# Optimization experiments

Hardware: AMD Instinct MI355X
Metric: run time of the kernel (lower is better)

## Reference

```python
import jax, jax.numpy as jnp
import numpy as np

TOPK = 50

def setup_inputs() -> dict:
    key = jax.random.key(0)
    k1, k2, k3, k4 = jax.random.split(key, 4)
    B, C, H, W = 8, 64, 256, 256
    x = jax.random.normal(k1, (B, C, H, W), dtype=jnp.float32)
    w_qkv = jax.random.normal(k2, (3 * C, C), dtype=jnp.float32) * 0.05
    w_proj = jax.random.normal(k3, (C, C), dtype=jnp.float32) * 0.05
    b_proj = jax.random.normal(k4, (C,), dtype=jnp.float32) * 0.05
    return {"x": x, "w_qkv": w_qkv, "w_proj": w_proj, "b_proj": b_proj}

def reference(x, w_qkv, w_proj, b_proj):
    B, C, H, W = x.shape
    N = H * W
    scale = C ** -0.5  # num_heads = 1, head_dim = C
    # NOTE: torch does x.reshape(B, N, C) on a (B,C,H,W) tensor -> raw
    # row-major reinterpretation; jnp.reshape matches this exactly.
    xf = x.reshape(B, N, C)
    qkv = xf @ w_qkv.T                                # (B, N, 3C)
    qkv = qkv.reshape(B, N, 3, 1, C).transpose(2, 0, 3, 1, 4)
    q, k, v = qkv[0], qkv[1], qkv[2]                  # each (B, 1, N, C)
    # channel attention: v^T @ k -> (B, 1, C, C)
    attn = jnp.einsum('bhnc,bhnd->bhcd', v, k) * scale
    # top-k mask along last dim (scatter of ones at top-k indices)
    _, idx = jax.lax.top_k(attn, TOPK)                # (B, 1, C, TOPK)
    mask = jax.nn.one_hot(idx, C, dtype=jnp.bool_).any(axis=-2)  # (B,1,C,C)
    attn = jnp.where(mask, attn, -jnp.inf)
    attn = jax.nn.softmax(attn, axis=-1)
    # attn @ q^T -> (B, 1, C, N), then raw reshape to (B, N, C) as in torch
    out = jnp.einsum('bhcd,bhnd->bhcn', attn, q).reshape(B, N, C)
    out = out @ w_proj.T + b_proj
    return out.reshape(B, C, H, W) + x
```

## Files before the change

kernel.cpp:

```cpp
#include <hip/hip_runtime.h>
#include <hip/hip_bf16.h>


#define BATCHES 8
#define NROWS 65536
#define CDIM 64
#define BATCH_FLOATS (NROWS * CDIM)

typedef __attribute__((ext_vector_type(8))) short bf16x8;
typedef __attribute__((ext_vector_type(4))) float f32x4;

__device__ __forceinline__ short f2bf(float f) {
    union { __hip_bfloat16 h; short s; } u;
    u.h = __float2bfloat16(f);
    return u.s;
}
__device__ __forceinline__ unsigned int pk2(float a, float b) {
    return (unsigned int)(unsigned short)f2bf(a) |
           ((unsigned int)(unsigned short)f2bf(b) << 16);
}

__device__ __forceinline__ void fma16g(float a, const float* __restrict__ p, float* acc) {
#pragma unroll
    for (int k = 0; k < 16; ++k) acc[k] = fmaf(a, p[k], acc[k]);
}
__device__ __forceinline__ void fma16v(float a, const float4* p, float* acc) {
    float4 b0 = p[0], b1 = p[1], b2 = p[2], b3 = p[3];
    acc[0]  = fmaf(a, b0.x, acc[0]);  acc[1]  = fmaf(a, b0.y, acc[1]);
    acc[2]  = fmaf(a, b0.z, acc[2]);  acc[3]  = fmaf(a, b0.w, acc[3]);
    acc[4]  = fmaf(a, b1.x, acc[4]);  acc[5]  = fmaf(a, b1.y, acc[5]);
    acc[6]  = fmaf(a, b1.z, acc[6]);  acc[7]  = fmaf(a, b1.w, acc[7]);
    acc[8]  = fmaf(a, b2.x, acc[8]);  acc[9]  = fmaf(a, b2.y, acc[9]);
    acc[10] = fmaf(a, b2.z, acc[10]); acc[11] = fmaf(a, b2.w, acc[11]);
    acc[12] = fmaf(a, b3.x, acc[12]); acc[13] = fmaf(a, b3.y, acc[13]);
    acc[14] = fmaf(a, b3.z, acc[14]); acc[15] = fmaf(a, b3.w, acc[15]);
}

__global__ __launch_bounds__(256) void k1_gram(const float* __restrict__ x,
                                               float* __restrict__ Gpart,
                                               int ntiles) {
    __shared__ __align__(16) short xt[2][64 * 72];
    int p = blockIdx.x, b = blockIdx.y;
    int tid = threadIdx.x;
    int l = tid & 63;
    int w = tid >> 6;
    int lm = l & 15, q = l >> 4;
    int n0 = 4 * (tid >> 4);
    int c0 = tid & 15;
    const float* xb = x + (size_t)b * BATCH_FLOATS + (size_t)p * ntiles * 4096;

    f32x4 acc[4];
#pragma unroll
    for (int mi = 0; mi < 4; ++mi) acc[mi] = (f32x4){0.f, 0.f, 0.f, 0.f};

    float pre[4][4];
#pragma unroll
    for (int r = 0; r < 4; ++r)
#pragma unroll
        for (int i = 0; i < 4; ++i)
            pre[r][i] = xb[(size_t)(n0 + r) * 64 + c0 + 16 * i];

    for (int tt = 0; tt < ntiles; ++tt) {
        short* buf = xt[tt & 1];
#pragma unroll
        for (int i = 0; i < 4; ++i) {
            int f = c0 + 16 * i;
            uint2 pk;
            pk.x = pk2(pre[0][i], pre[1][i]);
            pk.y = pk2(pre[2][i], pre[3][i]);
            *(uint2*)&buf[f * 72 + n0] = pk;
        }
        if (tt + 1 < ntiles) {
            const float* nx = xb + (size_t)(tt + 1) * 4096;
#pragma unroll
            for (int r = 0; r < 4; ++r)
#pragma unroll
                for (int i = 0; i < 4; ++i)
                    pre[r][i] = nx[(size_t)(n0 + r) * 64 + c0 + 16 * i];
        }
        __syncthreads();
        bf16x8 bfrag[2];
#pragma unroll
        for (int ks = 0; ks < 2; ++ks)
            bfrag[ks] = *(const bf16x8*)&buf[(16 * w + lm) * 72 + ks * 32 + q * 8];
#pragma unroll
        for (int mi = 0; mi < 4; ++mi) {
#pragma unroll
            for (int ks = 0; ks < 2; ++ks) {
                bf16x8 af = *(const bf16x8*)&buf[(mi * 16 + lm) * 72 + ks * 32 + q * 8];
                acc[mi] = __builtin_amdgcn_mfma_f32_16x16x32_bf16(af, bfrag[ks], acc[mi], 0, 0, 0);
            }
        }
    }
    float* Gp = Gpart + ((size_t)(b * 64 + p) << 12);
#pragma unroll
    for (int mi = 0; mi < 4; ++mi)
#pragma unroll
        for (int r = 0; r < 4; ++r)
            Gp[(mi * 16 + q * 4 + r) * 64 + 16 * w + lm] = acc[mi][r];
}

#define S68 68
__global__ __launch_bounds__(256) void k2_attn(const float* __restrict__ Gpart,
                                               const float* __restrict__ w_qkv,
                                               const float* __restrict__ w_proj,
                                               ushort* __restrict__ m_bf,
                                               ushort* __restrict__ wpb) {
    __shared__ float A[64 * S68];
    __shared__ float Bf[64 * S68];
    __shared__ float Cf[64 * S68];
    int b = blockIdx.x;
    int tid = threadIdx.x;
    int lane = tid & 63;
    int w = __builtin_amdgcn_readfirstlane(tid >> 6);

    if (tid < 128) {
        int idx = b * 128 + tid;
        float4 v = ((const float4*)w_proj)[idx];
        uint2 pp;
        pp.x = pk2(v.x, v.y);
        pp.y = pk2(v.z, v.w);
        *(uint2*)(wpb + 4 * idx) = pp;
    }

    {
        const float* gp = Gpart + ((size_t)b * 64 << 12);
        float4 s[4];
#pragma unroll
        for (int u = 0; u < 4; ++u) s[u] = make_float4(0.f, 0.f, 0.f, 0.f);
#pragma unroll 4
        for (int p = 0; p < 64; ++p) {
            const float4* g4 = (const float4*)(gp + ((size_t)p << 12));
#pragma unroll
            for (int u = 0; u < 4; ++u) {
                float4 v = g4[u * 256 + tid];
                s[u].x += v.x; s[u].y += v.y; s[u].z += v.z; s[u].w += v.w;
            }
        }
#pragma unroll
        for (int u = 0; u < 4; ++u) {
            int idx = u * 256 + tid;
            int c = idx >> 4, f = (idx & 15) * 4;
            A[c * S68 + f + 0] = s[u].x; A[c * S68 + f + 1] = s[u].y;
            A[c * S68 + f + 2] = s[u].z; A[c * S68 + f + 3] = s[u].w;
        }
    }
#pragma unroll
    for (int u = 0; u < 4; ++u) {
        int idx = u * 256 + tid;
        int d = idx >> 4, f = (idx & 15) * 4;
        float4 kv = ((const float4*)(w_qkv + 64 * 64))[idx];
        Bf[(f + 0) * S68 + d] = kv.x; Bf[(f + 1) * S68 + d] = kv.y;
        Bf[(f + 2) * S68 + d] = kv.z; Bf[(f + 3) * S68 + d] = kv.w;
        float4 vv = ((const float4*)(w_qkv + 128 * 64))[idx];
        Cf[(f + 0) * S68 + d] = vv.x; Cf[(f + 1) * S68 + d] = vv.y;
        Cf[(f + 2) * S68 + d] = vv.z; Cf[(f + 3) * S68 + d] = vv.w;
    }
    __syncthreads();

    float acc[16];
#pragma unroll
    for (int k = 0; k < 16; ++k) acc[k] = 0.f;
    for (int f = 0; f < 64; ++f)
        fma16v(A[f * S68 + lane], (const float4*)&Bf[f * S68 + 16 * w], acc);
    __syncthreads();
#pragma unroll
    for (int k = 0; k < 16; ++k) A[lane * S68 + 16 * w + k] = acc[k];
    __syncthreads();

#pragma unroll
    for (int k = 0; k < 16; ++k) acc[k] = 0.f;
    for (int e = 0; e < 64; ++e)
        fma16v(Cf[e * S68 + lane], (const float4*)&A[e * S68 + 16 * w], acc);
#pragma unroll
    for (int k = 0; k < 16; ++k) Bf[lane * S68 + 16 * w + k] = acc[k] * 0.125f;
    __syncthreads();

#pragma unroll 1
    for (int k = 0; k < 16; ++k) {
        int c = 16 * w + k;
        float v = Bf[c * S68 + lane];
        int rank = 0;
#pragma unroll
        for (int d4 = 0; d4 < 16; ++d4) {
            float4 vv = *(const float4*)&Bf[c * S68 + 4 * d4];
            rank += (vv.x > v) || (vv.x == v && (4 * d4 + 0) < lane);
            rank += (vv.y > v) || (vv.y == v && (4 * d4 + 1) < lane);
            rank += (vv.z > v) || (vv.z == v && (4 * d4 + 2) < lane);
            rank += (vv.w > v) || (vv.w == v && (4 * d4 + 3) < lane);
        }
        bool act = rank < 50;
        float mv = act ? v : -INFINITY;
#pragma unroll
        for (int s = 1; s < 64; s <<= 1) mv = fmaxf(mv, __shfl_xor(mv, s, 64));
        float e = act ? expf(v - mv) : 0.f;
        float sum = e;
#pragma unroll
        for (int s = 1; s < 64; s <<= 1) sum += __shfl_xor(sum, s, 64);
        Cf[lane * S68 + c] = e / sum;
    }
    __syncthreads();

#pragma unroll
    for (int k = 0; k < 16; ++k) acc[k] = 0.f;
    for (int d = 0; d < 64; ++d)
        fma16g(Cf[d * S68 + lane], w_qkv + d * 64 + 16 * w, acc);
    unsigned int uu[8];
#pragma unroll
    for (int i = 0; i < 8; ++i)
        uu[i] = pk2(acc[2 * i], acc[2 * i + 1]);
    ushort* dst = m_bf + (size_t)b * 4096 + lane * 64 + 16 * w;
    *(uint4*)dst = make_uint4(uu[0], uu[1], uu[2], uu[3]);
    *(uint4*)(dst + 8) = make_uint4(uu[4], uu[5], uu[6], uu[7]);
}

__global__ __launch_bounds__(256) void k3_main(const float* __restrict__ x,
                                               const ushort* __restrict__ m_bf,
                                               const ushort* __restrict__ wpb,
                                               const float* __restrict__ b_proj,
                                               float* __restrict__ out) {
    __shared__ __align__(16) short xt[64 * 64];
    __shared__ __align__(16) short yyt[64 * 64];
    int t = blockIdx.x, b = blockIdx.y;
    int tid = threadIdx.x;
    int l = tid & 63;
    int w = tid >> 6;
    int lm = l & 15, q = l >> 4;
    const float* xb = x + (size_t)b * BATCH_FLOATS;

    int rowbase = (16 * w + lm) * 1024 + t;
    const float* xr = xb + (size_t)rowbase * 64 + q * 4;
    float4 resid[4];
#pragma unroll
    for (int mi = 0; mi < 4; ++mi) resid[mi] = *(const float4*)(xr + mi * 16);

    const ushort* mb = m_bf + (size_t)b * 4096;
    bf16x8 b1[2];
#pragma unroll
    for (int ks = 0; ks < 2; ++ks)
        b1[ks] = *(const bf16x8*)(mb + (16 * w + lm) * 64 + ks * 32 + q * 8);

    {
        const float4* s = (const float4*)(xb + (size_t)(64 * t) * 64);
#pragma unroll
        for (int u = 0; u < 4; ++u) {
            float4 v = s[u * 256 + tid];
            int row = u * 16 + (tid >> 4);
            int colb = (tid & 15) * 8;
            int off = row * 128 + (colb ^ ((row & 7) << 4));
            uint2 p;
            p.x = pk2(v.x, v.y);
            p.y = pk2(v.z, v.w);
            *(uint2*)((char*)xt + off) = p;
        }
    }
    __syncthreads();

    f32x4 acc1[4];
#pragma unroll
    for (int mi = 0; mi < 4; ++mi) {
        acc1[mi] = (f32x4){0.f, 0.f, 0.f, 0.f};
#pragma unroll
        for (int ks = 0; ks < 2; ++ks) {
            int row = mi * 16 + lm;
            bf16x8 af = *(const bf16x8*)((const char*)xt + row * 128 +
                                         ((ks * 64 + q * 16) ^ ((lm & 7) << 4)));
            acc1[mi] = __builtin_amdgcn_mfma_f32_16x16x32_bf16(af, b1[ks], acc1[mi], 0, 0, 0);
        }
    }
    {
        int r = 16 * w + lm;
#pragma unroll
        for (int mi = 0; mi < 4; ++mi) {
            uint2 p;
            p.x = pk2(acc1[mi][0], acc1[mi][1]);
            p.y = pk2(acc1[mi][2], acc1[mi][3]);
            int off = r * 128 + (((mi * 32) + (q * 8)) ^ ((r & 7) << 4));
            *(uint2*)((char*)yyt + off) = p;
        }
    }

    bf16x8 b2[2];
    {
        int r = 16 * w + lm;
#pragma unroll
        for (int ks = 0; ks < 2; ++ks)
            b2[ks] = *(const bf16x8*)((const char*)yyt + r * 128 +
                                      ((ks * 64 + q * 16) ^ ((r & 7) << 4)));
    }
    f32x4 acc2[4];
#pragma unroll
    for (int mi = 0; mi < 4; ++mi) {
        acc2[mi] = (f32x4){0.f, 0.f, 0.f, 0.f};
#pragma unroll
        for (int ks = 0; ks < 2; ++ks) {
            bf16x8 af = *(const bf16x8*)(wpb + (mi * 16 + lm) * 64 + ks * 32 + q * 8);
            acc2[mi] = __builtin_amdgcn_mfma_f32_16x16x32_bf16(af, b2[ks], acc2[mi], 0, 0, 0);
        }
    }

    float* ob = out + (size_t)b * BATCH_FLOATS + (size_t)rowbase * 64 + q * 4;
#pragma unroll
    for (int mi = 0; mi < 4; ++mi) {
        float4 bias = *(const float4*)(b_proj + mi * 16 + q * 4);
        float4 o;
        o.x = acc2[mi][0] + bias.x + resid[mi].x;
        o.y = acc2[mi][1] + bias.y + resid[mi].y;
        o.z = acc2[mi][2] + bias.z + resid[mi].z;
        o.w = acc2[mi][3] + bias.w + resid[mi].w;
        *(float4*)(ob + mi * 16) = o;
    }
}

extern "C" void kernel_launch(void* const* d_in, const int* in_sizes, int n_in,
                              void* d_out, int out_size, void* d_ws, size_t ws_size,
                              hipStream_t stream) {
    (void)in_sizes; (void)n_in; (void)out_size; (void)ws_size;
    const float* x      = (const float*)d_in[0];
    const float* w_qkv  = (const float*)d_in[1];
    const float* w_proj = (const float*)d_in[2];
    const float* b_proj = (const float*)d_in[3];
    float* out = (float*)d_out;
    float* ws  = (float*)d_ws;

    float*  Gpart = ws;
    ushort* m_bf  = (ushort*)(ws + 8 * 64 * 4096);
    ushort* wpb   = m_bf + 8 * 4096;

    k1_gram<<<dim3(64, BATCHES), 256, 0, stream>>>(x, Gpart, 16);
    k2_attn<<<BATCHES, 256, 0, stream>>>(Gpart, w_qkv, w_proj, m_bf, wpb);
    k3_main<<<dim3(1024, BATCHES), 256, 0, stream>>>(x, m_bf, wpb, b_proj, out);
}
```

Measured before the change: 361.6 us.

## Compute Q projection in gram kernel and split Gpart reduction into separate kernel

Result: slower. 386.3 us (+6.8%).

```diff
diff --git a/kernel.cpp b/kernel.cpp
--- a/kernel.cpp
+++ b/kernel.cpp
@@ -20,10 +20,6 @@
            ((unsigned int)(unsigned short)f2bf(b) << 16);
 }
 
-__device__ __forceinline__ void fma16g(float a, const float* __restrict__ p, float* acc) {
-#pragma unroll
-    for (int k = 0; k < 16; ++k) acc[k] = fmaf(a, p[k], acc[k]);
-}
 __device__ __forceinline__ void fma16v(float a, const float4* p, float* acc) {
     float4 b0 = p[0], b1 = p[1], b2 = p[2], b3 = p[3];
     acc[0]  = fmaf(a, b0.x, acc[0]);  acc[1]  = fmaf(a, b0.y, acc[1]);
@@ -37,9 +33,12 @@
 }
 
 __global__ __launch_bounds__(256) void k1_gram(const float* __restrict__ x,
+                                               const float* __restrict__ w_qkv,
                                                float* __restrict__ Gpart,
+                                               ushort* __restrict__ Qw,
                                                int ntiles) {
     __shared__ __align__(16) short xt[2][64 * 72];
+    __shared__ __align__(16) short xr[2][64 * 72];
     int p = blockIdx.x, b = blockIdx.y;
     int tid = threadIdx.x;
     int l = tid & 63;
@@ -48,6 +47,18 @@
     int n0 = 4 * (tid >> 4);
     int c0 = tid & 15;
     const float* xb = x + (size_t)b * BATCH_FLOATS + (size_t)p * ntiles * 4096;
+    ushort* Qb = Qw + (size_t)b * BATCH_FLOATS + (size_t)p * ntiles * 4096;
+
+    bf16x8 wqf[2];
+#pragma unroll
+    for (int ks = 0; ks < 2; ++ks) {
+        const float* wp = w_qkv + (16 * w + lm) * 64 + ks * 32 + q * 8;
+        float4 a0 = *(const float4*)wp, a1 = *(const float4*)(wp + 4);
+        bf16x8 f;
+        f[0] = f2bf(a0.x); f[1] = f2bf(a0.y); f[2] = f2bf(a0.z); f[3] = f2bf(a0.w);
+        f[4] = f2bf(a1.x); f[5] = f2bf(a1.y); f[6] = f2bf(a1.z); f[7] = f2bf(a1.w);
+        wqf[ks] = f;
+    }
 
     f32x4 acc[4];
 #pragma unroll
@@ -62,6 +73,7 @@
 
     for (int tt = 0; tt < ntiles; ++tt) {
         short* buf = xt[tt & 1];
+        short* bufr = xr[tt & 1];
 #pragma unroll
         for (int i = 0; i < 4; ++i) {
             int f = c0 + 16 * i;
@@ -69,6 +81,9 @@
             pk.x = pk2(pre[0][i], pre[1][i]);
             pk.y = pk2(pre[2][i], pre[3][i]);
             *(uint2*)&buf[f * 72 + n0] = pk;
+#pragma unroll
+            for (int r = 0; r < 4; ++r)
+                bufr[(n0 + r) * 72 + f] = f2bf(pre[r][i]);
         }
         if (tt + 1 < ntiles) {
             const float* nx = xb + (size_t)(tt + 1) * 4096;
@@ -91,6 +106,19 @@
                 acc[mi] = __builtin_amdgcn_mfma_f32_16x16x32_bf16(af, bfrag[ks], acc[mi], 0, 0, 0);
             }
         }
+#pragma unroll
+        for (int mi = 0; mi < 4; ++mi) {
+            f32x4 aq = (f32x4){0.f, 0.f, 0.f, 0.f};
+#pragma unroll
+            for (int ks = 0; ks < 2; ++ks) {
+                bf16x8 af = *(const bf16x8*)&bufr[(mi * 16 + lm) * 72 + ks * 32 + q * 8];
+                aq = __builtin_amdgcn_mfma_f32_16x16x32_bf16(af, wqf[ks], aq, 0, 0, 0);
+            }
+            ushort* qd = Qb + (size_t)(tt * 64 + mi * 16 + q * 4) * 64 + 16 * w + lm;
+#pragma unroll
+            for (int r = 0; r < 4; ++r)
+                qd[r * 64] = (ushort)f2bf(aq[r]);
+        }
     }
     float* Gp = Gpart + ((size_t)(b * 64 + p) << 12);
 #pragma unroll
@@ -100,11 +128,22 @@
             Gp[(mi * 16 + q * 4 + r) * 64 + 16 * w + lm] = acc[mi][r];
 }
 
+__global__ __launch_bounds__(256) void k1b_reduce(const float* __restrict__ Gpart,
+                                                  float* __restrict__ G) {
+    int b = blockIdx.y;
+    int e = blockIdx.x * 256 + threadIdx.x;
+    const float* gp = Gpart + ((size_t)(b * 64) << 12) + e;
+    float s = 0.f;
+#pragma unroll 8
+    for (int pp = 0; pp < 64; ++pp) s += gp[(size_t)pp << 12];
+    G[b * 4096 + e] = s;
+}
+
 #define S68 68
-__global__ __launch_bounds__(256) void k2_attn(const float* __restrict__ Gpart,
+__global__ __launch_bounds__(256) void k2_attn(const float* __restrict__ G,
                                                const float* __restrict__ w_qkv,
                                                const float* __restrict__ w_proj,
-                                               ushort* __restrict__ m_bf,
+                                               ushort* __restrict__ a_bf,
                                                ushort* __restrict__ wpb) {
     __shared__ float A[64 * S68];
     __shared__ float Bf[64 * S68];
@@ -124,25 +163,14 @@
     }
 
     {
-        const float* gp = Gpart + ((size_t)b * 64 << 12);
-        float4 s[4];
-#pragma unroll
-        for (int u = 0; u < 4; ++u) s[u] = make_float4(0.f, 0.f, 0.f, 0.f);
-#pragma unroll 4
-        for (int p = 0; p < 64; ++p) {
-            const float4* g4 = (const float4*)(gp + ((size_t)p << 12));
-#pragma unroll
-            for (int u = 0; u < 4; ++u) {
-                float4 v = g4[u * 256 + tid];
-                s[u].x += v.x; s[u].y += v.y; s[u].z += v.z; s[u].w += v.w;
-            }
-        }
+        const float4* g4 = (const float4*)(G + b * 4096);
 #pragma unroll
         for (int u = 0; u < 4; ++u) {
             int idx = u * 256 + tid;
             int c = idx >> 4, f = (idx & 15) * 4;
-            A[c * S68 + f + 0] = s[u].x; A[c * S68 + f + 1] = s[u].y;
-            A[c * S68 + f + 2] = s[u].z; A[c * S68 + f + 3] = s[u].w;
+            float4 g = g4[idx];
+            A[c * S68 + f + 0] = g.x; A[c * S68 + f + 1] = g.y;
+            A[c * S68 + f + 2] = g.z; A[c * S68 + f + 3] = g.w;
         }
     }
 #pragma unroll
@@ -176,6 +204,7 @@
     for (int k = 0; k < 16; ++k) Bf[lane * S68 + 16 * w + k] = acc[k] * 0.125f;
     __syncthreads();
 
+    ushort* ab = a_bf + (size_t)b * 4096;
 #pragma unroll 1
     for (int k = 0; k < 16; ++k) {
         int c = 16 * w + k;
@@ -197,29 +226,16 @@
         float sum = e;
 #pragma unroll
         for (int s = 1; s < 64; s <<= 1) sum += __shfl_xor(sum, s, 64);
-        Cf[lane * S68 + c] = e / sum;
-    }
-    __syncthreads();
-
-#pragma unroll
-    for (int k = 0; k < 16; ++k) acc[k] = 0.f;
-    for (int d = 0; d < 64; ++d)
-        fma16g(Cf[d * S68 + lane], w_qkv + d * 64 + 16 * w, acc);
-    unsigned int uu[8];
-#pragma unroll
-    for (int i = 0; i < 8; ++i)
-        uu[i] = pk2(acc[2 * i], acc[2 * i + 1]);
-    ushort* dst = m_bf + (size_t)b * 4096 + lane * 64 + 16 * w;
-    *(uint4*)dst = make_uint4(uu[0], uu[1], uu[2], uu[3]);
-    *(uint4*)(dst + 8) = make_uint4(uu[4], uu[5], uu[6], uu[7]);
+        ab[c * 64 + lane] = (ushort)f2bf(e / sum);
+    }
 }
 
 __global__ __launch_bounds__(256) void k3_main(const float* __restrict__ x,
-                                               const ushort* __restrict__ m_bf,
+                                               const ushort* __restrict__ Qw,
+                                               const ushort* __restrict__ a_bf,
                                                const ushort* __restrict__ wpb,
                                                const float* __restrict__ b_proj,
                                                float* __restrict__ out) {
-    __shared__ __align__(16) short xt[64 * 64];
     __shared__ __align__(16) short yyt[64 * 64];
     int t = blockIdx.x, b = blockIdx.y;
     int tid = threadIdx.x;
@@ -234,37 +250,20 @@
 #pragma unroll
     for (int mi = 0; mi < 4; ++mi) resid[mi] = *(const float4*)(xr + mi * 16);
 
-    const ushort* mb = m_bf + (size_t)b * 4096;
+    const ushort* ab = a_bf + (size_t)b * 4096;
     bf16x8 b1[2];
 #pragma unroll
     for (int ks = 0; ks < 2; ++ks)
-        b1[ks] = *(const bf16x8*)(mb + (16 * w + lm) * 64 + ks * 32 + q * 8);
-
-    {
-        const float4* s = (const float4*)(xb + (size_t)(64 * t) * 64);
-#pragma unroll
-        for (int u = 0; u < 4; ++u) {
-            float4 v = s[u * 256 + tid];
-            int row = u * 16 + (tid >> 4);
-            int colb = (tid & 15) * 8;
-            int off = row * 128 + (colb ^ ((row & 7) << 4));
-            uint2 p;
-            p.x = pk2(v.x, v.y);
-            p.y = pk2(v.z, v.w);
-            *(uint2*)((char*)xt + off) = p;
-        }
-    }
-    __syncthreads();
-
+        b1[ks] = *(const bf16x8*)(ab + (16 * w + lm) * 64 + ks * 32 + q * 8);
+
+    const ushort* Qt = Qw + (size_t)b * BATCH_FLOATS + (size_t)(64 * t) * 64;
     f32x4 acc1[4];
 #pragma unroll
     for (int mi = 0; mi < 4; ++mi) {
         acc1[mi] = (f32x4){0.f, 0.f, 0.f, 0.f};
 #pragma unroll
         for (int ks = 0; ks < 2; ++ks) {
-            int row = mi * 16 + lm;
-            bf16x8 af = *(const bf16x8*)((const char*)xt + row * 128 +
-                                         ((ks * 64 + q * 16) ^ ((lm & 7) << 4)));
+            bf16x8 af = *(const bf16x8*)(Qt + (size_t)(mi * 16 + lm) * 64 + ks * 32 + q * 8);
             acc1[mi] = __builtin_amdgcn_mfma_f32_16x16x32_bf16(af, b1[ks], acc1[mi], 0, 0, 0);
         }
     }
@@ -321,13 +320,16 @@
     const float* w_proj = (const float*)d_in[2];
     const float* b_proj = (const float*)d_in[3];
     float* out = (float*)d_out;
-    float* ws  = (float*)d_ws;
-
-    float*  Gpart = ws;
-    ushort* m_bf  = (ushort*)(ws + 8 * 64 * 4096);
-    ushort* wpb   = m_bf + 8 * 4096;
-
-    k1_gram<<<dim3(64, BATCHES), 256, 0, stream>>>(x, Gpart, 16);
-    k2_attn<<<BATCHES, 256, 0, stream>>>(Gpart, w_qkv, w_proj, m_bf, wpb);
-    k3_main<<<dim3(1024, BATCHES), 256, 0, stream>>>(x, m_bf, wpb, b_proj, out);
-}
+    char*  ws  = (char*)d_ws;
+
+    float*  Gpart = (float*)(ws);
+    ushort* Qw    = (ushort*)(ws + (8u << 20));
+    float*  G     = (float*)(ws + (72u << 20));
+    ushort* a_bf  = (ushort*)(ws + (72u << 20) + (128u << 10));
+    ushort* wpb   = a_bf + BATCHES * 4096;
+
+    k1_gram<<<dim3(64, BATCHES), 256, 0, stream>>>(x, w_qkv, Gpart, Qw, 16);
+    k1b_reduce<<<dim3(16, BATCHES), 256, 0, stream>>>(Gpart, G);
+    k2_attn<<<BATCHES, 256, 0, stream>>>(G, w_qkv, w_proj, a_bf, wpb);
+    k3_main<<<dim3(1024, BATCHES), 256, 0, stream>>>(x, Qw, a_bf, wpb, b_proj, out);
+}
```

## Split Gram partial reduction into separate kernel and widen attention block to 1024 threads

Applied to the files above, without the earlier changes.

Result: faster. 320.4 us (-11.4%).

```diff
diff --git a/kernel.cpp b/kernel.cpp
--- a/kernel.cpp
+++ b/kernel.cpp
@@ -18,22 +18,6 @@
 __device__ __forceinline__ unsigned int pk2(float a, float b) {
     return (unsigned int)(unsigned short)f2bf(a) |
            ((unsigned int)(unsigned short)f2bf(b) << 16);
-}
-
-__device__ __forceinline__ void fma16g(float a, const float* __restrict__ p, float* acc) {
-#pragma unroll
-    for (int k = 0; k < 16; ++k) acc[k] = fmaf(a, p[k], acc[k]);
-}
-__device__ __forceinline__ void fma16v(float a, const float4* p, float* acc) {
-    float4 b0 = p[0], b1 = p[1], b2 = p[2], b3 = p[3];
-    acc[0]  = fmaf(a, b0.x, acc[0]);  acc[1]  = fmaf(a, b0.y, acc[1]);
-    acc[2]  = fmaf(a, b0.z, acc[2]);  acc[3]  = fmaf(a, b0.w, acc[3]);
-    acc[4]  = fmaf(a, b1.x, acc[4]);  acc[5]  = fmaf(a, b1.y, acc[5]);
-    acc[6]  = fmaf(a, b1.z, acc[6]);  acc[7]  = fmaf(a, b1.w, acc[7]);
-    acc[8]  = fmaf(a, b2.x, acc[8]);  acc[9]  = fmaf(a, b2.y, acc[9]);
-    acc[10] = fmaf(a, b2.z, acc[10]); acc[11] = fmaf(a, b2.w, acc[11]);
-    acc[12] = fmaf(a, b3.x, acc[12]); acc[13] = fmaf(a, b3.y, acc[13]);
-    acc[14] = fmaf(a, b3.z, acc[14]); acc[15] = fmaf(a, b3.w, acc[15]);
 }
 
 __global__ __launch_bounds__(256) void k1_gram(const float* __restrict__ x,
@@ -100,19 +84,30 @@
             Gp[(mi * 16 + q * 4 + r) * 64 + 16 * w + lm] = acc[mi][r];
 }
 
+__global__ __launch_bounds__(256) void k1b_reduce(const float* __restrict__ Gpart,
+                                                  float* __restrict__ G) {
+    int b = blockIdx.y;
+    int e = blockIdx.x * 256 + threadIdx.x;
+    const float* gp = Gpart + ((size_t)(b * 64) << 12) + e;
+    float s = 0.f;
+#pragma unroll 8
+    for (int pp = 0; pp < 64; ++pp) s += gp[(size_t)pp << 12];
+    G[b * 4096 + e] = s;
+}
+
 #define S68 68
-__global__ __launch_bounds__(256) void k2_attn(const float* __restrict__ Gpart,
-                                               const float* __restrict__ w_qkv,
-                                               const float* __restrict__ w_proj,
-                                               ushort* __restrict__ m_bf,
-                                               ushort* __restrict__ wpb) {
+__global__ __launch_bounds__(1024) void k2_attn(const float* __restrict__ G,
+                                                const float* __restrict__ w_qkv,
+                                                const float* __restrict__ w_proj,
+                                                ushort* __restrict__ m_bf,
+                                                ushort* __restrict__ wpb) {
     __shared__ float A[64 * S68];
     __shared__ float Bf[64 * S68];
     __shared__ float Cf[64 * S68];
     int b = blockIdx.x;
     int tid = threadIdx.x;
     int lane = tid & 63;
-    int w = __builtin_amdgcn_readfirstlane(tid >> 6);
+    int wg = tid >> 6;
 
     if (tid < 128) {
         int idx = b * 128 + tid;
@@ -124,31 +119,12 @@
     }
 
     {
-        const float* gp = Gpart + ((size_t)b * 64 << 12);
-        float4 s[4];
-#pragma unroll
-        for (int u = 0; u < 4; ++u) s[u] = make_float4(0.f, 0.f, 0.f, 0.f);
-#pragma unroll 4
-        for (int p = 0; p < 64; ++p) {
-            const float4* g4 = (const float4*)(gp + ((size_t)p << 12));
-#pragma unroll
-            for (int u = 0; u < 4; ++u) {
-                float4 v = g4[u * 256 + tid];
-                s[u].x += v.x; s[u].y += v.y; s[u].z += v.z; s[u].w += v.w;
-            }
-        }
-#pragma unroll
-        for (int u = 0; u < 4; ++u) {
-            int idx = u * 256 + tid;
-            int c = idx >> 4, f = (idx & 15) * 4;
-            A[c * S68 + f + 0] = s[u].x; A[c * S68 + f + 1] = s[u].y;
-            A[c * S68 + f + 2] = s[u].z; A[c * S68 + f + 3] = s[u].w;
-        }
-    }
-#pragma unroll
-    for (int u = 0; u < 4; ++u) {
-        int idx = u * 256 + tid;
-        int d = idx >> 4, f = (idx & 15) * 4;
+        int idx = tid;
+        int c = idx >> 4, f = (idx & 15) * 4;
+        float4 g = ((const float4*)(G + b * 4096))[idx];
+        A[c * S68 + f + 0] = g.x; A[c * S68 + f + 1] = g.y;
+        A[c * S68 + f + 2] = g.z; A[c * S68 + f + 3] = g.w;
+        int d = idx >> 4;
         float4 kv = ((const float4*)(w_qkv + 64 * 64))[idx];
         Bf[(f + 0) * S68 + d] = kv.x; Bf[(f + 1) * S68 + d] = kv.y;
         Bf[(f + 2) * S68 + d] = kv.z; Bf[(f + 3) * S68 + d] = kv.w;
@@ -158,27 +134,35 @@
     }
     __syncthreads();
 
-    float acc[16];
-#pragma unroll
-    for (int k = 0; k < 16; ++k) acc[k] = 0.f;
-    for (int f = 0; f < 64; ++f)
-        fma16v(A[f * S68 + lane], (const float4*)&Bf[f * S68 + 16 * w], acc);
-    __syncthreads();
-#pragma unroll
-    for (int k = 0; k < 16; ++k) A[lane * S68 + 16 * w + k] = acc[k];
-    __syncthreads();
-
-#pragma unroll
-    for (int k = 0; k < 16; ++k) acc[k] = 0.f;
-    for (int e = 0; e < 64; ++e)
-        fma16v(Cf[e * S68 + lane], (const float4*)&A[e * S68 + 16 * w], acc);
-#pragma unroll
-    for (int k = 0; k < 16; ++k) Bf[lane * S68 + 16 * w + k] = acc[k] * 0.125f;
-    __syncthreads();
-
-#pragma unroll 1
-    for (int k = 0; k < 16; ++k) {
-        int c = 16 * w + k;
+    float acc[4] = {0.f, 0.f, 0.f, 0.f};
+    for (int f = 0; f < 64; ++f) {
+        float a = A[f * S68 + lane];
+        float4 bv = *(const float4*)&Bf[f * S68 + 4 * wg];
+        acc[0] = fmaf(a, bv.x, acc[0]);
+        acc[1] = fmaf(a, bv.y, acc[1]);
+        acc[2] = fmaf(a, bv.z, acc[2]);
+        acc[3] = fmaf(a, bv.w, acc[3]);
+    }
+    __syncthreads();
+    *(float4*)&A[lane * S68 + 4 * wg] = make_float4(acc[0], acc[1], acc[2], acc[3]);
+    __syncthreads();
+
+    acc[0] = acc[1] = acc[2] = acc[3] = 0.f;
+    for (int e = 0; e < 64; ++e) {
+        float a = Cf[e * S68 + lane];
+        float4 bv = *(const float4*)&A[e * S68 + 4 * wg];
+        acc[0] = fmaf(a, bv.x, acc[0]);
+        acc[1] = fmaf(a, bv.y, acc[1]);
+        acc[2] = fmaf(a, bv.z, acc[2]);
+        acc[3] = fmaf(a, bv.w, acc[3]);
+    }
+    *(float4*)&Bf[lane * S68 + 4 * wg] = make_float4(acc[0] * 0.125f, acc[1] * 0.125f,
+                                                     acc[2] * 0.125f, acc[3] * 0.125f);
+    __syncthreads();
+
+#pragma unroll
+    for (int k = 0; k < 4; ++k) {
+        int c = 4 * wg + k;
         float v = Bf[c * S68 + lane];
         int rank = 0;
 #pragma unroll
@@ -201,17 +185,19 @@
     }
     __syncthreads();
 
-#pragma unroll
-    for (int k = 0; k < 16; ++k) acc[k] = 0.f;
-    for (int d = 0; d < 64; ++d)
-        fma16g(Cf[d * S68 + lane], w_qkv + d * 64 + 16 * w, acc);
-    unsigned int uu[8];
-#pragma unroll
-    for (int i = 0; i < 8; ++i)
-        uu[i] = pk2(acc[2 * i], acc[2 * i + 1]);
-    ushort* dst = m_bf + (size_t)b * 4096 + lane * 64 + 16 * w;
-    *(uint4*)dst = make_uint4(uu[0], uu[1], uu[2], uu[3]);
-    *(uint4*)(dst + 8) = make_uint4(uu[4], uu[5], uu[6], uu[7]);
+    acc[0] = acc[1] = acc[2] = acc[3] = 0.f;
+    for (int d = 0; d < 64; ++d) {
+        float a = Cf[d * S68 + lane];
+        float4 wv4 = *(const float4*)(w_qkv + d * 64 + 4 * wg);
+        acc[0] = fmaf(a, wv4.x, acc[0]);
+        acc[1] = fmaf(a, wv4.y, acc[1]);
+        acc[2] = fmaf(a, wv4.z, acc[2]);
+        acc[3] = fmaf(a, wv4.w, acc[3]);
+    }
+    uint2 pp;
+    pp.x = pk2(acc[0], acc[1]);
+    pp.y = pk2(acc[2], acc[3]);
+    *(uint2*)(m_bf + (size_t)b * 4096 + lane * 64 + 4 * wg) = pp;
 }
 
 __global__ __launch_bounds__(256) void k3_main(const float* __restrict__ x,
@@ -321,13 +307,15 @@
     const float* w_proj = (const float*)d_in[2];
     const float* b_proj = (const float*)d_in[3];
     float* out = (float*)d_out;
-    float* ws  = (float*)d_ws;
-
-    float*  Gpart = ws;
-    ushort* m_bf  = (ushort*)(ws + 8 * 64 * 4096);
-    ushort* wpb   = m_bf + 8 * 4096;
+    char*  ws  = (char*)d_ws;
+
+    float*  Gpart = (float*)(ws);
+    float*  G     = (float*)(ws + (8u << 20));
+    ushort* m_bf  = (ushort*)(ws + (8u << 20) + (128u << 10));
+    ushort* wpb   = m_bf + BATCHES * 4096;
 
     k1_gram<<<dim3(64, BATCHES), 256, 0, stream>>>(x, Gpart, 16);
-    k2_attn<<<BATCHES, 256, 0, stream>>>(Gpart, w_qkv, w_proj, m_bf, wpb);
+    k1b_reduce<<<dim3(16, BATCHES), 256, 0, stream>>>(Gpart, G);
+    k2_attn<<<BATCHES, 1024, 0, stream>>>(G, w_qkv, w_proj, m_bf, wpb);
     k3_main<<<dim3(1024, BATCHES), 256, 0, stream>>>(x, m_bf, wpb, b_proj, out);
 }
```
